# Optimization experiments

Hardware: AMD Instinct MI355X
Metric: run time of the kernel (lower is better)

## Reference

```python
import jax, jax.numpy as jnp
import numpy as np

EMBED_DIM = 384
NUM_HEADS = 6
HEAD_DIM = EMBED_DIM // NUM_HEADS
MLP_HIDDEN = 4 * EMBED_DIM
LN_EPS = 1e-5


def layer_norm(x, gamma, beta):
    mu = jnp.mean(x, axis=-1, keepdims=True)
    var = jnp.mean((x - mu) ** 2, axis=-1, keepdims=True)
    return (x - mu) * jax.lax.rsqrt(var + LN_EPS) * gamma + beta


def setup_inputs() -> dict:
    key = jax.random.key(0)
    ks = jax.random.split(key, 8)
    D, H = EMBED_DIM, MLP_HIDDEN
    s = 1.0 / np.sqrt(D)
    sh = 1.0 / np.sqrt(H)
    return {
        "x": jax.random.normal(ks[0], (16, 1024, D), dtype=jnp.float32),
        "ln1_g": jnp.ones((D,), jnp.float32),
        "ln1_b": jnp.zeros((D,), jnp.float32),
        "qkv_w": jax.random.uniform(ks[1], (3 * D, D), jnp.float32, -s, s),
        "qkv_b": jax.random.uniform(ks[2], (3 * D,), jnp.float32, -s, s),
        "proj_w": jax.random.uniform(ks[3], (D, D), jnp.float32, -s, s),
        "proj_b": jax.random.uniform(ks[4], (D,), jnp.float32, -s, s),
        "ln2_g": jnp.ones((D,), jnp.float32),
        "ln2_b": jnp.zeros((D,), jnp.float32),
        "fc1_w": jax.random.uniform(ks[5], (H, D), jnp.float32, -s, s),
        "fc1_b": jax.random.uniform(ks[6], (H,), jnp.float32, -s, s),
        "fc2_w": jax.random.uniform(ks[7], (D, H), jnp.float32, -sh, sh),
        "fc2_b": jnp.zeros((D,), jnp.float32),
    }


def reference(x, ln1_g, ln1_b, qkv_w, qkv_b, proj_w, proj_b,
              ln2_g, ln2_b, fc1_w, fc1_b, fc2_w, fc2_b):
    B, N, D = x.shape
    Hh, Dh = NUM_HEADS, HEAD_DIM
    scale = Dh ** -0.5

    # --- attention sublayer (pre-norm) ---
    h = layer_norm(x, ln1_g, ln1_b)
    qkv = h @ qkv_w.T + qkv_b                      # [B,N,3D]
    qkv = qkv.reshape(B, N, 3, Hh, Dh)
    q, k, v = (qkv[:, :, i].transpose(0, 2, 1, 3) for i in range(3))  # [B,H,N,Dh]
    attn = jax.nn.softmax(jnp.einsum('bhnd,bhmd->bhnm', q, k) * scale, axis=-1)
    o = jnp.einsum('bhnm,bhmd->bhnd', attn, v)     # [B,H,N,Dh]
    o = o.transpose(0, 2, 1, 3).reshape(B, N, D)
    x = x + (o @ proj_w.T + proj_b)

    # --- MLP sublayer (pre-norm) ---
    h = layer_norm(x, ln2_g, ln2_b)
    h = jax.nn.gelu(h @ fc1_w.T + fc1_b, approximate=False)
    x = x + (h @ fc2_w.T + fc2_b)
    return x
```

## Files before the change

### kernel.cpp

```cpp
#include <hip/hip_runtime.h>

typedef unsigned short u16;
typedef unsigned int   u32;
typedef __bf16  bf16x8 __attribute__((ext_vector_type(8)));
typedef __bf16  bf16x4_t __attribute__((ext_vector_type(4)));
typedef float   f32x4  __attribute__((ext_vector_type(4)));
typedef float   f32x2  __attribute__((ext_vector_type(2)));

struct Ptrs { const void* p[13]; };

extern "C" __device__ float __ocml_native_exp2_f32(float);

__device__ __forceinline__ float bf2f(u16 u) {
    union { unsigned int i; float f; } c; c.i = ((unsigned int)u) << 16; return c.f;
}
__device__ __forceinline__ u16 f2bf(float f) {
    union { float f; unsigned int i; } c; c.f = f;
    unsigned int u = c.i;
    unsigned int r = (u + 0x7fffu + ((u >> 16) & 1u)) >> 16;
    return (u16)r;
}

__device__ __forceinline__ float wave_sum(float x) {
#pragma unroll
    for (int m = 32; m >= 1; m >>= 1) x += __shfl_xor(x, m);
    return x;
}

__device__ __forceinline__ void g2l16(const u16* g, u16* l) {
    __builtin_amdgcn_global_load_lds(
        (__attribute__((address_space(1))) void*)g,
        (__attribute__((address_space(3))) void*)l, 16, 0, 0);
}

__global__ void k_flag(const u32* __restrict__ w, int* __restrict__ flagp)
{
    if (threadIdx.x == 0) {
        int cnt = 0;
        for (int i = 0; i < 128; ++i) {
            u16 lo = (u16)(w[i] & 0xFFFFu);
            int e = (lo >> 7) & 0xFF;
            cnt += (e >= 117 && e <= 123) ? 1 : 0;
        }
        *flagp = (cnt >= 64) ? 1 : 0;
    }
}

__global__ __launch_bounds__(256) void k_convert(Ptrs ps,
                                                 u16* __restrict__ cw,
                                                 const int* __restrict__ flagp)
{
    const int cum[13] = {0,48,96,55392,55536,73968,74016,74064,74112,
                         147840,148032,221760,221808};
    const int off[12] = {0,384,768,443136,444288,591744,
                         592128,592512,592896,1182720,1184256,1774080};
    int c = blockIdx.x * 256 + threadIdx.x;
    if (c >= 221808) return;
    int seg = 0;
#pragma unroll
    for (int i = 1; i < 12; ++i) seg += (c >= cum[i]) ? 1 : 0;
    int e = (c - cum[seg]) * 8;
    u16* dst = cw + off[seg] + e;
    if (*flagp) {
        *(uint4*)dst = *((const uint4*)ps.p[seg + 1] + (e >> 3));
    } else {
        const float* s = (const float*)ps.p[seg + 1] + e;
        u16 tmp[8];
#pragma unroll
        for (int t = 0; t < 8; ++t) tmp[t] = f2bf(s[t]);
        *(uint4*)dst = *(const uint4*)tmp;
    }
}

__global__ __launch_bounds__(256) void k_ln1cvt(const void* __restrict__ xin,
                                                const u16* __restrict__ g,
                                                const u16* __restrict__ b,
                                                u16* __restrict__ cx,
                                                u16* __restrict__ h,
                                                const int* __restrict__ flagp)
{
    const int wid = threadIdx.x >> 6, lane = threadIdx.x & 63;
    const int row = blockIdx.x * 4 + wid;
    const int e0 = lane * 6;
    float v[6]; u16 raw[6];
    if (*flagp) {
        const u16* p = (const u16*)xin + (size_t)row * 384 + e0;
        u32 w0 = *(const u32*)(p);
        u32 w1 = *(const u32*)(p + 2);
        u32 w2 = *(const u32*)(p + 4);
        raw[0] = (u16)w0; raw[1] = (u16)(w0 >> 16);
        raw[2] = (u16)w1; raw[3] = (u16)(w1 >> 16);
        raw[4] = (u16)w2; raw[5] = (u16)(w2 >> 16);
#pragma unroll
        for (int t = 0; t < 6; t++) v[t] = bf2f(raw[t]);
    } else {
        const float* p = (const float*)xin + (size_t)row * 384 + e0;
        f32x2 a0 = *(const f32x2*)(p);
        f32x2 a1 = *(const f32x2*)(p + 2);
        f32x2 a2 = *(const f32x2*)(p + 4);
        v[0] = a0[0]; v[1] = a0[1]; v[2] = a1[0];
        v[3] = a1[1]; v[4] = a2[0]; v[5] = a2[1];
#pragma unroll
        for (int t = 0; t < 6; t++) raw[t] = f2bf(v[t]);
    }
    u32* pc = (u32*)(cx + (size_t)row * 384 + e0);
    pc[0] = (u32)raw[0] | ((u32)raw[1] << 16);
    pc[1] = (u32)raw[2] | ((u32)raw[3] << 16);
    pc[2] = (u32)raw[4] | ((u32)raw[5] << 16);
    float s = 0.f;
#pragma unroll
    for (int t = 0; t < 6; t++) s += v[t];
    const float mu = wave_sum(s) * (1.0f / 384.0f);
    float vs = 0.f;
#pragma unroll
    for (int t = 0; t < 6; t++) { float d = v[t] - mu; vs += d * d; }
    const float var = wave_sum(vs) * (1.0f / 384.0f);
    const float rs = rsqrtf(var + 1e-5f);
    const u32* gg = (const u32*)(g + e0);
    const u32* bb = (const u32*)(b + e0);
    u32 gw[3] = {gg[0], gg[1], gg[2]};
    u32 bw[3] = {bb[0], bb[1], bb[2]};
    u16 ow[6];
#pragma unroll
    for (int t = 0; t < 6; t++) {
        u16 ge = (u16)(gw[t >> 1] >> ((t & 1) * 16));
        u16 be = (u16)(bw[t >> 1] >> ((t & 1) * 16));
        ow[t] = f2bf((v[t] - mu) * rs * bf2f(ge) + bf2f(be));
    }
    u32* po = (u32*)(h + (size_t)row * 384 + e0);
    po[0] = (u32)ow[0] | ((u32)ow[1] << 16);
    po[1] = (u32)ow[2] | ((u32)ow[3] << 16);
    po[2] = (u32)ow[4] | ((u32)ow[5] << 16);
}

__device__ __forceinline__ void gemm_core_128(const u16* __restrict__ A,
                                              const u16* __restrict__ B,
                                              int K, int m0, int n0,
                                              f32x4 (&acc)[4][4])
{
    __shared__ __align__(16) u16 As[128 * 64];
    __shared__ __align__(16) u16 Bs[128 * 64];

    const int tid  = threadIdx.x;
    const int lane = tid & 63;
    const int wid  = tid >> 6;
    const int wm  = (wid >> 1) * 64;
    const int wn  = (wid & 1) * 64;
    const int l15 = lane & 15;
    const int g   = lane >> 4;
    const int srow   = lane >> 3;
    const int schunk = ((lane & 7) ^ srow) * 8;

    const u16* Abase = A + (size_t)(m0 + wid * 32 + srow) * K + schunk;
    const u16* Bbase = B + (size_t)(n0 + wid * 32 + srow) * K + schunk;

    for (int kk = 0; kk < K; kk += 64) {
        __syncthreads();
#pragma unroll
        for (int t = 0; t < 4; ++t) {
            g2l16(Abase + (size_t)t * 8 * K + kk, &As[(wid * 32 + t * 8) * 64]);
            g2l16(Bbase + (size_t)t * 8 * K + kk, &Bs[(wid * 32 + t * 8) * 64]);
        }
        __syncthreads();

#pragma unroll
        for (int ks = 0; ks < 2; ++ks) {
            bf16x8 af[4], bfr[4];
#pragma unroll
            for (int i = 0; i < 4; i++) {
                int row = wm + 16 * i + l15;
                int p = ((ks * 4 + g) ^ (l15 & 7)) * 8;
                af[i] = __builtin_bit_cast(bf16x8,
                         *(const uint4*)&As[row * 64 + p]);
            }
#pragma unroll
            for (int j = 0; j < 4; j++) {
                int row = wn + 16 * j + l15;
                int p = ((ks * 4 + g) ^ (l15 & 7)) * 8;
                bfr[j] = __builtin_bit_cast(bf16x8,
                         *(const uint4*)&Bs[row * 64 + p]);
            }
#pragma unroll
            for (int i = 0; i < 4; i++)
#pragma unroll
                for (int j = 0; j < 4; j++)
                    acc[i][j] = __builtin_amdgcn_mfma_f32_16x16x32_bf16(
                                    af[i], bfr[j], acc[i][j], 0, 0, 0);
        }
    }
}

__device__ __forceinline__ void gemm_core_128x64(const u16* __restrict__ A,
                                                 const u16* __restrict__ B,
                                                 int K, int m0, int n0,
                                                 f32x4 (&acc)[4][2])
{
    __shared__ __align__(16) u16 As[128 * 64];
    __shared__ __align__(16) u16 Bs[64 * 64];

    const int tid  = threadIdx.x;
    const int lane = tid & 63;
    const int wid  = tid >> 6;
    const int wm  = (wid >> 1) * 64;
    const int wn  = (wid & 1) * 32;
    const int l15 = lane & 15;
    const int g   = lane >> 4;
    const int srow   = lane >> 3;
    const int schunk = ((lane & 7) ^ srow) * 8;

    const u16* Abase = A + (size_t)(m0 + wid * 32 + srow) * K + schunk;
    const u16* Bbase = B + (size_t)(n0 + wid * 16 + srow) * K + schunk;

    for (int kk = 0; kk < K; kk += 64) {
        __syncthreads();
#pragma unroll
        for (int t = 0; t < 4; ++t)
            g2l16(Abase + (size_t)t * 8 * K + kk, &As[(wid * 32 + t * 8) * 64]);
#pragma unroll
        for (int t = 0; t < 2; ++t)
            g2l16(Bbase + (size_t)t * 8 * K + kk, &Bs[(wid * 16 + t * 8) * 64]);
        __syncthreads();

#pragma unroll
        for (int ks = 0; ks < 2; ++ks) {
            bf16x8 af[4], bfr[2];
#pragma unroll
            for (int i = 0; i < 4; i++) {
                int row = wm + 16 * i + l15;
                int p = ((ks * 4 + g) ^ (l15 & 7)) * 8;
                af[i] = __builtin_bit_cast(bf16x8,
                         *(const uint4*)&As[row * 64 + p]);
            }
#pragma unroll
            for (int j = 0; j < 2; j++) {
                int row = wn + 16 * j + l15;
                int p = ((ks * 4 + g) ^ (l15 & 7)) * 8;
                bfr[j] = __builtin_bit_cast(bf16x8,
                         *(const uint4*)&Bs[row * 64 + p]);
            }
#pragma unroll
            for (int i = 0; i < 4; i++)
#pragma unroll
                for (int j = 0; j < 2; j++)
                    acc[i][j] = __builtin_amdgcn_mfma_f32_16x16x32_bf16(
                                    af[i], bfr[j], acc[i][j], 0, 0, 0);
        }
    }
}

__global__ __launch_bounds__(256) void k_layernorm(const u16* __restrict__ in,
                                                   const u16* __restrict__ g,
                                                   const u16* __restrict__ b,
                                                   u16* __restrict__ out,
                                                   int nrows)
{
    const int wid = threadIdx.x >> 6, lane = threadIdx.x & 63;
    const int row = blockIdx.x * 4 + wid;
    if (row >= nrows) return;
    const int e0 = lane * 6;
    float v[6];
    const u16* p = in + (size_t)row * 384 + e0;
    u32 w0 = *(const u32*)(p);
    u32 w1 = *(const u32*)(p + 2);
    u32 w2 = *(const u32*)(p + 4);
    v[0] = bf2f((u16)w0); v[1] = bf2f((u16)(w0 >> 16));
    v[2] = bf2f((u16)w1); v[3] = bf2f((u16)(w1 >> 16));
    v[4] = bf2f((u16)w2); v[5] = bf2f((u16)(w2 >> 16));
    float s = 0.f;
#pragma unroll
    for (int t = 0; t < 6; t++) s += v[t];
    const float mu = wave_sum(s) * (1.0f / 384.0f);
    float vs = 0.f;
#pragma unroll
    for (int t = 0; t < 6; t++) { float d = v[t] - mu; vs += d * d; }
    const float var = wave_sum(vs) * (1.0f / 384.0f);
    const float rs = rsqrtf(var + 1e-5f);
    const u32* gg = (const u32*)(g + e0);
    const u32* bb = (const u32*)(b + e0);
    u32 gw[3] = {gg[0], gg[1], gg[2]};
    u32 bw[3] = {bb[0], bb[1], bb[2]};
    u16 ow[6];
#pragma unroll
    for (int t = 0; t < 6; t++) {
        u16 ge = (u16)(gw[t >> 1] >> ((t & 1) * 16));
        u16 be = (u16)(bw[t >> 1] >> ((t & 1) * 16));
        ow[t] = f2bf((v[t] - mu) * rs * bf2f(ge) + bf2f(be));
    }
    u32* po = (u32*)(out + (size_t)row * 384 + e0);
    po[0] = (u32)ow[0] | ((u32)ow[1] << 16);
    po[1] = (u32)ow[2] | ((u32)ow[3] << 16);
    po[2] = (u32)ow[4] | ((u32)ow[5] << 16);
}

__global__ __launch_bounds__(256) void k_gemm_qkv(const u16* __restrict__ A,
                                                  const u16* __restrict__ W,
                                                  const u16* __restrict__ bias,
                                                  u16* __restrict__ q,
                                                  u16* __restrict__ k,
                                                  u16* __restrict__ vrow)
{
    const int id = blockIdx.x, slot = id & 7, idx = id >> 3;
    const int m0 = (slot * 16 + idx / 9) * 128;
    const int n0 = (idx % 9) * 128;
    f32x4 acc[4][4];
#pragma unroll
    for (int i = 0; i < 4; i++)
#pragma unroll
        for (int j = 0; j < 4; j++) acc[i][j] = f32x4{0.f, 0.f, 0.f, 0.f};
    gemm_core_128(A, W, 384, m0, n0, acc);
    const int lane = threadIdx.x & 63, wid = threadIdx.x >> 6;
    const int wm = (wid >> 1) * 64, wn = (wid & 1) * 64;
    const int l15 = lane & 15, rq = (lane >> 4) * 4;
#pragma unroll
    for (int i = 0; i < 4; i++)
#pragma unroll
        for (int j = 0; j < 4; j++)
#pragma unroll
            for (int r = 0; r < 4; r++) {
                int gr = m0 + wm + 16 * i + rq + r;
                int gc = n0 + wn + 16 * j + l15;
                float v = acc[i][j][r] + bf2f(bias[gc]);
                int part = gc / 384, rem = gc % 384;
                int head = rem >> 6, dh = rem & 63;
                int bb = gr >> 10, nn = gr & 1023;
                int bh = bb * 6 + head;
                u16* dst = (part == 0) ? q : (part == 1) ? k : vrow;
                dst[((size_t)bh * 1024 + nn) * 64 + dh] = f2bf(v);
            }
}

__global__ __launch_bounds__(256) void k_transpose_v(const u16* __restrict__ v,
                                                     u16* __restrict__ vT)
{
    __shared__ u16 T[64 * 72];
    const int bh = blockIdx.y, n0 = blockIdx.x * 64;
    const int tid = threadIdx.x;
    const int r = tid >> 2;
    const int c = (tid & 3) * 16;
    const u16* src = v + (size_t)bh * 65536 + (size_t)(n0 + r) * 64 + c;
    uint4 a = *(const uint4*)src;
    uint4 b = *(const uint4*)(src + 8);
    u16 buf[16];
    *(uint4*)&buf[0] = a; *(uint4*)&buf[8] = b;
#pragma unroll
    for (int e = 0; e < 16; ++e) T[(c + e) * 72 + r] = buf[e];
    __syncthreads();
    uint4 o0 = *(const uint4*)&T[r * 72 + c];
    uint4 o1 = *(const uint4*)&T[r * 72 + c + 8];
    u16* dst = vT + (size_t)bh * 65536 + (size_t)r * 1024 + n0 + c;
    *(uint4*)dst = o0;
    *(uint4*)(dst + 8) = o1;
}

__global__ __launch_bounds__(256) void k_attn(const u16* __restrict__ q,
                                              const u16* __restrict__ kk,
                                              const u16* __restrict__ vT,
                                              u16* __restrict__ o)
{
    __shared__ __align__(16) u16 Ks[128 * 64];
    __shared__ __align__(16) u16 Vs[2][64 * 64];
    __shared__ __align__(16) u16 Ps[128 * 64];

    const int tid = threadIdx.x, lane = tid & 63, wid = tid >> 6;
    const int l15 = lane & 15, g = lane >> 4, q8 = g * 8;
    const int id = blockIdx.x;
    const int bh = (id & 7) * 12 + ((id >> 3) >> 3);
    const int q0 = ((id >> 3) & 7) * 128;
    const int wrow = wid * 32;

    const u16* Q = q  + (size_t)bh * 65536;
    const u16* K = kk + (size_t)bh * 65536;
    const u16* V = vT + (size_t)bh * 65536;

    const int srow   = lane >> 3;
    const int schunk = ((lane & 7) ^ srow) * 8;
    const int rd0 = ((0 + g) ^ (l15 & 7)) * 8;
    const int rd1 = ((4 + g) ^ (l15 & 7)) * 8;
    int pcol[4];
#pragma unroll
    for (int ip = 0; ip < 4; ++ip)
        pcol[ip] = (((ip * 2 + (g >> 1)) ^ (l15 & 7)) * 8) + (g & 1) * 4;

    bf16x8 aq[2][2];
#pragma unroll
    for (int jp = 0; jp < 2; ++jp)
#pragma unroll
        for (int ks = 0; ks < 2; ++ks) {
            bf16x8 t = __builtin_bit_cast(bf16x8,
                *(const uint4*)&Q[(size_t)(q0 + wrow + jp * 16 + l15) * 64
                                  + ks * 32 + q8]);
#pragma unroll
            for (int e = 0; e < 8; ++e)
                t[e] = (__bf16)((float)t[e] * 0.18033688f);
            aq[jp][ks] = t;
        }

    f32x4 ob[2][4];
#pragma unroll
    for (int i = 0; i < 2; ++i)
#pragma unroll
        for (int j = 0; j < 4; ++j) ob[i][j] = f32x4{0.f, 0.f, 0.f, 0.f};
    float lsum[2] = {0.f, 0.f};

    for (int kt2 = 0; kt2 < 8; ++kt2) {
        __syncthreads();
#pragma unroll
        for (int t = 0; t < 4; ++t) {
            int r0 = wid * 32 + t * 8;
            g2l16(&K[(size_t)(kt2 * 128 + r0 + srow) * 64 + schunk], &Ks[r0 * 64]);
        }
#pragma unroll
        for (int h = 0; h < 2; ++h)
#pragma unroll
            for (int t = 0; t < 2; ++t) {
                int r0 = wid * 16 + t * 8;
                g2l16(&V[(size_t)(r0 + srow) * 1024 + kt2 * 128 + h * 64 + schunk],
                      &Vs[h][r0 * 64]);
            }
        __syncthreads();

#pragma unroll 1
        for (int h = 0; h < 2; ++h) {
            f32x4 st[4][2];
#pragma unroll
            for (int ip = 0; ip < 4; ++ip)
#pragma unroll
                for (int jp = 0; jp < 2; ++jp) st[ip][jp] = f32x4{0.f,0.f,0.f,0.f};
            __builtin_amdgcn_s_setprio(1);
#pragma unroll
            for (int ip = 0; ip < 4; ++ip) {
                int rbase = (h * 64 + ip * 16 + l15) * 64;
                bf16x8 bk0 = __builtin_bit_cast(bf16x8,
                    *(const uint4*)&Ks[rbase + rd0]);
                bf16x8 bk1 = __builtin_bit_cast(bf16x8,
                    *(const uint4*)&Ks[rbase + rd1]);
#pragma unroll
                for (int jp = 0; jp < 2; ++jp) {
                    st[ip][jp] = __builtin_amdgcn_mfma_f32_16x16x32_bf16(
                                    bk0, aq[jp][0], st[ip][jp], 0, 0, 0);
                    st[ip][jp] = __builtin_amdgcn_mfma_f32_16x16x32_bf16(
                                    bk1, aq[jp][1], st[ip][jp], 0, 0, 0);
                }
            }
            __builtin_amdgcn_s_setprio(0);

#pragma unroll
            for (int jp = 0; jp < 2; ++jp) {
                float ps = 0.f;
#pragma unroll
                for (int ip = 0; ip < 4; ++ip)
#pragma unroll
                    for (int r = 0; r < 4; ++r) {
                        float p = __ocml_native_exp2_f32(st[ip][jp][r]);
                        st[ip][jp][r] = p;
                        ps += p;
                    }
                lsum[jp] += ps;
            }

#pragma unroll
            for (int ip = 0; ip < 4; ++ip)
#pragma unroll
                for (int jp = 0; jp < 2; ++jp) {
                    bf16x4_t pk;
#pragma unroll
                    for (int r = 0; r < 4; ++r) pk[r] = (__bf16)st[ip][jp][r];
                    *(bf16x4_t*)&Ps[(wrow + jp*16 + l15) * 64 + pcol[ip]] = pk;
                }

            __builtin_amdgcn_s_setprio(1);
#pragma unroll
            for (int ks = 0; ks < 2; ++ks) {
                const int rdo = ks ? rd1 : rd0;
                bf16x8 ap[2];
#pragma unroll
                for (int i = 0; i < 2; ++i)
                    ap[i] = __builtin_bit_cast(bf16x8,
                        *(const uint4*)&Ps[(wrow + i*16 + l15) * 64 + rdo]);
#pragma unroll
                for (int jv = 0; jv < 4; ++jv) {
                    bf16x8 bv = __builtin_bit_cast(bf16x8,
                        *(const uint4*)&Vs[h][(jv * 16 + l15) * 64 + rdo]);
#pragma unroll
                    for (int i = 0; i < 2; ++i)
                        ob[i][jv] = __builtin_amdgcn_mfma_f32_16x16x32_bf16(
                                      ap[i], bv, ob[i][jv], 0, 0, 0);
                }
            }
            __builtin_amdgcn_s_setprio(0);
        }
    }

#pragma unroll
    for (int jp = 0; jp < 2; ++jp) {
        lsum[jp] += __shfl_xor(lsum[jp], 16);
        lsum[jp] += __shfl_xor(lsum[jp], 32);
    }
    const int bb = bh / 6, hh = bh % 6;
#pragma unroll
    for (int i = 0; i < 2; ++i)
#pragma unroll
        for (int r = 0; r < 4; ++r) {
            int src = (lane & 48) | (g * 4 + r);
            float linv = 1.0f / __shfl(lsum[i], src);
            int row = q0 + wrow + i * 16 + g * 4 + r;
#pragma unroll
            for (int jv = 0; jv < 4; ++jv) {
                int dh = jv * 16 + l15;
                o[((size_t)(bb * 1024 + row)) * 384 + hh * 64 + dh] =
                    f2bf(ob[i][jv][r] * linv);
            }
        }
}

__global__ __launch_bounds__(256) void k_gemm_proj(const u16* __restrict__ A,
                                                   const u16* __restrict__ W,
                                                   const u16* __restrict__ bias,
                                                   const u16* __restrict__ xin,
                                                   u16* __restrict__ x1)
{
    const int id = blockIdx.x, slot = id & 7, idx = id >> 3;
    const int m0 = (slot * 16 + idx / 6) * 128;
    const int n0 = (idx % 6) * 64;
    f32x4 acc[4][2];
#pragma unroll
    for (int i = 0; i < 4; i++)
#pragma unroll
        for (int j = 0; j < 2; j++) acc[i][j] = f32x4{0.f, 0.f, 0.f, 0.f};
    gemm_core_128x64(A, W, 384, m0, n0, acc);
    const int lane = threadIdx.x & 63, wid = threadIdx.x >> 6;
    const int wm = (wid >> 1) * 64, wn = (wid & 1) * 32;
    const int l15 = lane & 15, rq = (lane >> 4) * 4;
#pragma unroll
    for (int i = 0; i < 4; i++)
#pragma unroll
        for (int j = 0; j < 2; j++)
#pragma unroll
            for (int r = 0; r < 4; r++) {
                int gr = m0 + wm + 16 * i + rq + r;
                int gc = n0 + wn + 16 * j + l15;
                size_t ix = (size_t)gr * 384 + gc;
                x1[ix] = f2bf(acc[i][j][r] + bf2f(bias[gc]) + bf2f(xin[ix]));
            }
}

__global__ __launch_bounds__(256) void k_gemm_fc1(const u16* __restrict__ A,
                                                  const u16* __restrict__ W,
                                                  const u16* __restrict__ bias,
                                                  u16* __restrict__ hmid)
{
    const int id = blockIdx.x, slot = id & 7, idx = id >> 3;
    const int mbase = (slot * 8 + idx / 12) * 256;
    const int n0 = (idx % 12) * 128;
#pragma unroll 1
    for (int sub = 0; sub < 2; ++sub) {
        const int m0 = mbase + sub * 128;
        f32x4 acc[4][4];
#pragma unroll
        for (int i = 0; i < 4; i++)
#pragma unroll
            for (int j = 0; j < 4; j++) acc[i][j] = f32x4{0.f, 0.f, 0.f, 0.f};
        gemm_core_128(A, W, 384, m0, n0, acc);
        const int lane = threadIdx.x & 63, wid = threadIdx.x >> 6;
        const int wm = (wid >> 1) * 64, wn = (wid & 1) * 64;
        const int l15 = lane & 15, rq = (lane >> 4) * 4;
#pragma unroll
        for (int i = 0; i < 4; i++)
#pragma unroll
            for (int j = 0; j < 4; j++)
#pragma unroll
                for (int r = 0; r < 4; r++) {
                    int gr = m0 + wm + 16 * i + rq + r;
                    int gc = n0 + wn + 16 * j + l15;
                    float v = acc[i][j][r] + bf2f(bias[gc]);
                    float u = v * (1.5957691f + 0.0713548f * v * v);
                    float ge = v * __builtin_amdgcn_rcpf(1.0f + __expf(-u));
                    hmid[(size_t)gr * 1536 + gc] = f2bf(ge);
                }
    }
}

__global__ __launch_bounds__(256) void k_gemm_fc2(const u16* __restrict__ A,
                                                  const u16* __restrict__ W,
                                                  const u16* __restrict__ bias,
                                                  const u16* __restrict__ x1,
                                                  void* __restrict__ outv,
                                                  const int* __restrict__ flagp)
{
    const int id = blockIdx.x, slot = id & 7, idx = id >> 3;
    const int m0 = (slot * 16 + idx / 6) * 128;
    const int n0 = (idx % 6) * 64;
    f32x4 acc[4][2];
#pragma unroll
    for (int i = 0; i < 4; i++)
#pragma unroll
        for (int j = 0; j < 2; j++) acc[i][j] = f32x4{0.f, 0.f, 0.f, 0.f};
    gemm_core_128x64(A, W, 1536, m0, n0, acc);
    const int lane = threadIdx.x & 63, wid = threadIdx.x >> 6;
    const int wm = (wid >> 1) * 64, wn = (wid & 1) * 32;
    const int l15 = lane & 15, rq = (lane >> 4) * 4;
    const int isbf = *flagp;
    u16*   ob = (u16*)outv;
    float* of = (float*)outv;
#pragma unroll
    for (int i = 0; i < 4; i++)
#pragma unroll
        for (int j = 0; j < 2; j++)
#pragma unroll
            for (int r = 0; r < 4; r++) {
                int gr = m0 + wm + 16 * i + rq + r;
                int gc = n0 + wn + 16 * j + l15;
                size_t ix = (size_t)gr * 384 + gc;
                float v = acc[i][j][r] + bf2f(bias[gc]) + bf2f(x1[ix]);
                if (isbf) ob[ix] = f2bf(v);
                else      of[ix] = v;
            }
}

extern "C" void kernel_launch(void* const* d_in, const int* in_sizes, int n_in,
                              void* d_out, int out_size, void* d_ws, size_t ws_size,
                              hipStream_t stream)
{
    char* ws = (char*)d_ws;
    u16*   cw   = (u16*)(ws + 0);
    int*   flag = (int*)(ws + 3548928);
    u16*   cx   = (u16*)(ws + 3549184);
    u16*   h    = (u16*)(ws + 16132096);
    u16*   x1   = (u16*)(ws + 28715008);
    u16*   q    = (u16*)(ws + 53880832);
    u16*   kbuf = (u16*)(ws + 66463744);
    u16*   vT   = (u16*)(ws + 79046656);
    u16*   o    = (u16*)(ws + 91629568);
    u16*   vrow = o;
    u16*   hmid = (u16*)(ws + 53880832);

    const u16* c_ln1_g  = cw + 0;
    const u16* c_ln1_b  = cw + 384;
    const u16* c_qkv_w  = cw + 768;
    const u16* c_qkv_b  = cw + 443136;
    const u16* c_proj_w = cw + 444288;
    const u16* c_proj_b = cw + 591744;
    const u16* c_ln2_g  = cw + 592128;
    const u16* c_ln2_b  = cw + 592512;
    const u16* c_fc1_w  = cw + 592896;
    const u16* c_fc1_b  = cw + 1182720;
    const u16* c_fc2_w  = cw + 1184256;
    const u16* c_fc2_b  = cw + 1774080;

    Ptrs ps;
    for (int i = 0; i < 13; ++i) ps.p[i] = d_in[i];

    k_flag<<<1, 64, 0, stream>>>((const u32*)d_in[3], flag);
    k_convert<<<867, 256, 0, stream>>>(ps, cw, flag);
    k_ln1cvt<<<4096, 256, 0, stream>>>(d_in[0], c_ln1_g, c_ln1_b, cx, h, flag);
    k_gemm_qkv<<<1152, 256, 0, stream>>>(h, c_qkv_w, c_qkv_b, q, kbuf, vrow);
    k_transpose_v<<<dim3(16, 96), 256, 0, stream>>>(vrow, vT);
    k_attn<<<768, 256, 0, stream>>>(q, kbuf, vT, o);
    k_gemm_proj<<<768, 256, 0, stream>>>(o, c_proj_w, c_proj_b, cx, x1);
    k_layernorm<<<4096, 256, 0, stream>>>(x1, c_ln2_g, c_ln2_b, h, 16384);
    k_gemm_fc1<<<768, 256, 0, stream>>>(h, c_fc1_w, c_fc1_b, hmid);
    k_gemm_fc2<<<768, 256, 0, stream>>>(hmid, c_fc2_w, c_fc2_b, x1,
                                        d_out, flag);
    (void)in_sizes; (void)n_in; (void)out_size; (void)ws_size; (void)c_fc2_b;
}
```

Measured before the change: 271.4 us.

## Fuse V transpose into QKV epilogue, merge flag kernel, retile fc1 GEMM

The QKV GEMM epilogue now writes V directly in transposed layout using packed 4-element stores, which removes the separate transpose kernel and its round trip through global memory. The bf16-detection flag is now computed inside the convert kernel rather than in its own single-thread launch, which saves one launch. The fc1 GEMM becomes a single 256x128 tile with a custom LDS-staged MFMA loop and swizzled layout instead of two sequential 128x128 sub-tiles, so each B tile is loaded once and reused across more rows. The trade-off is higher register pressure (128 accumulator floats per thread), redundant flag sniffing in every convert thread, and strided transposed stores for V.

Result: no change. 271.4 us (+0.0%).

```diff
diff --git a/kernel.cpp b/kernel.cpp
--- a/kernel.cpp
+++ b/kernel.cpp
@@ -33,27 +33,26 @@
         (__attribute__((address_space(3))) void*)l, 16, 0, 0);
 }
 
-__global__ void k_flag(const u32* __restrict__ w, int* __restrict__ flagp)
-{
-    if (threadIdx.x == 0) {
-        int cnt = 0;
-        for (int i = 0; i < 128; ++i) {
-            u16 lo = (u16)(w[i] & 0xFFFFu);
-            int e = (lo >> 7) & 0xFF;
-            cnt += (e >= 117 && e <= 123) ? 1 : 0;
-        }
-        *flagp = (cnt >= 64) ? 1 : 0;
-    }
+__device__ __forceinline__ int sniff_bf16(const u32* __restrict__ w) {
+    int cnt = 0;
+    for (int i = 0; i < 128; ++i) {
+        u16 lo = (u16)(w[i] & 0xFFFFu);
+        int e = (lo >> 7) & 0xFF;
+        cnt += (e >= 117 && e <= 123) ? 1 : 0;
+    }
+    return (cnt >= 64) ? 1 : 0;
 }
 
 __global__ __launch_bounds__(256) void k_convert(Ptrs ps,
                                                  u16* __restrict__ cw,
-                                                 const int* __restrict__ flagp)
+                                                 int* __restrict__ flagp)
 {
     const int cum[13] = {0,48,96,55392,55536,73968,74016,74064,74112,
                          147840,148032,221760,221808};
     const int off[12] = {0,384,768,443136,444288,591744,
                          592128,592512,592896,1182720,1184256,1774080};
+    const int flag = sniff_bf16((const u32*)ps.p[3]);
+    if (blockIdx.x == 0 && threadIdx.x == 0) *flagp = flag;
     int c = blockIdx.x * 256 + threadIdx.x;
     if (c >= 221808) return;
     int seg = 0;
@@ -61,7 +60,7 @@
     for (int i = 1; i < 12; ++i) seg += (c >= cum[i]) ? 1 : 0;
     int e = (c - cum[seg]) * 8;
     u16* dst = cw + off[seg] + e;
-    if (*flagp) {
+    if (flag) {
         *(uint4*)dst = *((const uint4*)ps.p[seg + 1] + (e >> 3));
     } else {
         const float* s = (const float*)ps.p[seg + 1] + e;
@@ -296,8 +295,8 @@
                                                   const u16* __restrict__ W,
                                                   const u16* __restrict__ bias,
                                                   u16* __restrict__ q,
-                                                  u16* __restrict__ k,
-                                                  u16* __restrict__ vrow)
+                                                  u16* __restrict__ kbuf,
+                                                  u16* __restrict__ vT)
 {
     const int id = blockIdx.x, slot = id & 7, idx = id >> 3;
     const int m0 = (slot * 16 + idx / 9) * 128;
@@ -312,44 +311,31 @@
     const int wm = (wid >> 1) * 64, wn = (wid & 1) * 64;
     const int l15 = lane & 15, rq = (lane >> 4) * 4;
 #pragma unroll
-    for (int i = 0; i < 4; i++)
-#pragma unroll
-        for (int j = 0; j < 4; j++)
-#pragma unroll
-            for (int r = 0; r < 4; r++) {
-                int gr = m0 + wm + 16 * i + rq + r;
-                int gc = n0 + wn + 16 * j + l15;
-                float v = acc[i][j][r] + bf2f(bias[gc]);
-                int part = gc / 384, rem = gc % 384;
-                int head = rem >> 6, dh = rem & 63;
-                int bb = gr >> 10, nn = gr & 1023;
-                int bh = bb * 6 + head;
-                u16* dst = (part == 0) ? q : (part == 1) ? k : vrow;
-                dst[((size_t)bh * 1024 + nn) * 64 + dh] = f2bf(v);
-            }
-}
-
-__global__ __launch_bounds__(256) void k_transpose_v(const u16* __restrict__ v,
-                                                     u16* __restrict__ vT)
-{
-    __shared__ u16 T[64 * 72];
-    const int bh = blockIdx.y, n0 = blockIdx.x * 64;
-    const int tid = threadIdx.x;
-    const int r = tid >> 2;
-    const int c = (tid & 3) * 16;
-    const u16* src = v + (size_t)bh * 65536 + (size_t)(n0 + r) * 64 + c;
-    uint4 a = *(const uint4*)src;
-    uint4 b = *(const uint4*)(src + 8);
-    u16 buf[16];
-    *(uint4*)&buf[0] = a; *(uint4*)&buf[8] = b;
-#pragma unroll
-    for (int e = 0; e < 16; ++e) T[(c + e) * 72 + r] = buf[e];
-    __syncthreads();
-    uint4 o0 = *(const uint4*)&T[r * 72 + c];
-    uint4 o1 = *(const uint4*)&T[r * 72 + c + 8];
-    u16* dst = vT + (size_t)bh * 65536 + (size_t)r * 1024 + n0 + c;
-    *(uint4*)dst = o0;
-    *(uint4*)(dst + 8) = o1;
+    for (int i = 0; i < 4; i++) {
+        const int grb = m0 + wm + 16 * i + rq;
+        const int bb = grb >> 10, nn = grb & 1023;
+#pragma unroll
+        for (int j = 0; j < 4; j++) {
+            const int gc = n0 + wn + 16 * j + l15;
+            const int part = gc / 384, rem = gc % 384;
+            const int head = rem >> 6, dh = rem & 63;
+            const int bh = bb * 6 + head;
+            float vals[4];
+#pragma unroll
+            for (int r = 0; r < 4; r++) vals[r] = acc[i][j][r] + bf2f(bias[gc]);
+            if (part == 2) {
+                u32 lo = (u32)f2bf(vals[0]) | ((u32)f2bf(vals[1]) << 16);
+                u32 hi = (u32)f2bf(vals[2]) | ((u32)f2bf(vals[3]) << 16);
+                uint2 pk; pk.x = lo; pk.y = hi;
+                *(uint2*)&vT[((size_t)bh * 64 + dh) * 1024 + nn] = pk;
+            } else {
+                u16* dst = part ? kbuf : q;
+#pragma unroll
+                for (int r = 0; r < 4; r++)
+                    dst[((size_t)bh * 1024 + nn + r) * 64 + dh] = f2bf(vals[r]);
+            }
+        }
+    }
 }
 
 __global__ __launch_bounds__(256) void k_attn(const u16* __restrict__ q,
@@ -549,35 +535,72 @@
                                                   const u16* __restrict__ bias,
                                                   u16* __restrict__ hmid)
 {
+    __shared__ __align__(16) u16 As[256 * 64];
+    __shared__ __align__(16) u16 Bs[128 * 64];
+
     const int id = blockIdx.x, slot = id & 7, idx = id >> 3;
-    const int mbase = (slot * 8 + idx / 12) * 256;
+    const int m0 = (slot * 8 + idx / 12) * 256;
     const int n0 = (idx % 12) * 128;
-#pragma unroll 1
-    for (int sub = 0; sub < 2; ++sub) {
-        const int m0 = mbase + sub * 128;
-        f32x4 acc[4][4];
-#pragma unroll
-        for (int i = 0; i < 4; i++)
-#pragma unroll
-            for (int j = 0; j < 4; j++) acc[i][j] = f32x4{0.f, 0.f, 0.f, 0.f};
-        gemm_core_128(A, W, 384, m0, n0, acc);
-        const int lane = threadIdx.x & 63, wid = threadIdx.x >> 6;
-        const int wm = (wid >> 1) * 64, wn = (wid & 1) * 64;
-        const int l15 = lane & 15, rq = (lane >> 4) * 4;
-#pragma unroll
-        for (int i = 0; i < 4; i++)
-#pragma unroll
-            for (int j = 0; j < 4; j++)
-#pragma unroll
-                for (int r = 0; r < 4; r++) {
-                    int gr = m0 + wm + 16 * i + rq + r;
-                    int gc = n0 + wn + 16 * j + l15;
-                    float v = acc[i][j][r] + bf2f(bias[gc]);
-                    float u = v * (1.5957691f + 0.0713548f * v * v);
-                    float ge = v * __builtin_amdgcn_rcpf(1.0f + __expf(-u));
-                    hmid[(size_t)gr * 1536 + gc] = f2bf(ge);
-                }
-    }
+
+    const int tid = threadIdx.x, lane = tid & 63, wid = tid >> 6;
+    const int l15 = lane & 15, g = lane >> 4;
+    const int srow = lane >> 3;
+    const int schunk = ((lane & 7) ^ srow) * 8;
+
+    const u16* Abase = A + (size_t)(m0 + wid * 64 + srow) * 384 + schunk;
+    const u16* Bbase = W + (size_t)(n0 + wid * 32 + srow) * 384 + schunk;
+
+    f32x4 acc[4][8];
+#pragma unroll
+    for (int i = 0; i < 4; i++)
+#pragma unroll
+        for (int j = 0; j < 8; j++) acc[i][j] = f32x4{0.f, 0.f, 0.f, 0.f};
+
+    for (int kk = 0; kk < 384; kk += 64) {
+        __syncthreads();
+#pragma unroll
+        for (int t = 0; t < 8; ++t)
+            g2l16(Abase + (size_t)t * 8 * 384 + kk, &As[(wid * 64 + t * 8) * 64]);
+#pragma unroll
+        for (int t = 0; t < 4; ++t)
+            g2l16(Bbase + (size_t)t * 8 * 384 + kk, &Bs[(wid * 32 + t * 8) * 64]);
+        __syncthreads();
+
+#pragma unroll
+        for (int ks = 0; ks < 2; ++ks) {
+            const int p = ((ks * 4 + g) ^ (l15 & 7)) * 8;
+            bf16x8 af[4], bfr[8];
+#pragma unroll
+            for (int i = 0; i < 4; i++)
+                af[i] = __builtin_bit_cast(bf16x8,
+                    *(const uint4*)&As[(wid * 64 + 16 * i + l15) * 64 + p]);
+#pragma unroll
+            for (int j = 0; j < 8; j++)
+                bfr[j] = __builtin_bit_cast(bf16x8,
+                    *(const uint4*)&Bs[(16 * j + l15) * 64 + p]);
+#pragma unroll
+            for (int i = 0; i < 4; i++)
+#pragma unroll
+                for (int j = 0; j < 8; j++)
+                    acc[i][j] = __builtin_amdgcn_mfma_f32_16x16x32_bf16(
+                                    af[i], bfr[j], acc[i][j], 0, 0, 0);
+        }
+    }
+
+    const int rq = g * 4;
+#pragma unroll
+    for (int i = 0; i < 4; i++)
+#pragma unroll
+        for (int j = 0; j < 8; j++)
+#pragma unroll
+            for (int r = 0; r < 4; r++) {
+                int gr = m0 + wid * 64 + 16 * i + rq + r;
+                int gc = n0 + 16 * j + l15;
+                float v = acc[i][j][r] + bf2f(bias[gc]);
+                float u = v * (1.5957691f + 0.0713548f * v * v);
+                float ge = v * __builtin_amdgcn_rcpf(1.0f + __expf(-u));
+                hmid[(size_t)gr * 1536 + gc] = f2bf(ge);
+            }
 }
 
 __global__ __launch_bounds__(256) void k_gemm_fc2(const u16* __restrict__ A,
@@ -631,7 +654,6 @@
     u16*   kbuf = (u16*)(ws + 66463744);
     u16*   vT   = (u16*)(ws + 79046656);
     u16*   o    = (u16*)(ws + 91629568);
-    u16*   vrow = o;
     u16*   hmid = (u16*)(ws + 53880832);
 
     const u16* c_ln1_g  = cw + 0;
@@ -650,11 +672,9 @@
     Ptrs ps;
     for (int i = 0; i < 13; ++i) ps.p[i] = d_in[i];
 
-    k_flag<<<1, 64, 0, stream>>>((const u32*)d_in[3], flag);
     k_convert<<<867, 256, 0, stream>>>(ps, cw, flag);
     k_ln1cvt<<<4096, 256, 0, stream>>>(d_in[0], c_ln1_g, c_ln1_b, cx, h, flag);
-    k_gemm_qkv<<<1152, 256, 0, stream>>>(h, c_qkv_w, c_qkv_b, q, kbuf, vrow);
-    k_transpose_v<<<dim3(16, 96), 256, 0, stream>>>(vrow, vT);
+    k_gemm_qkv<<<1152, 256, 0, stream>>>(h, c_qkv_w, c_qkv_b, q, kbuf, vT);
     k_attn<<<768, 256, 0, stream>>>(q, kbuf, vT, o);
     k_gemm_proj<<<768, 256, 0, stream>>>(o, c_proj_w, c_proj_b, cx, x1);
     k_layernorm<<<4096, 256, 0, stream>>>(x1, c_ln2_g, c_ln2_b, h, 16384);
```
